# Kernel tuning notes

Measured on AMD Instinct MI355X. Metric: run time of the kernel, lower is better.

The kernel has to match this reference:

```python
import jax, jax.numpy as jnp
import numpy as np

B, C, H, W = 2, 256, 64, 64
NH = 4          # num_heads -> ch = C // NH = 64
G = 32          # GroupNorm groups (normalization(channels))
EPS = 1e-5


def setup_inputs() -> dict:
    key = jax.random.key(0)
    ks = jax.random.split(key, 7)
    s = 1.0 / np.sqrt(C).astype(np.float32)
    return {
        "x": jax.random.normal(ks[0], (B, C, H, W), jnp.float32),
        "gn_scale": 1.0 + 0.02 * jax.random.normal(ks[1], (C,), jnp.float32),
        "gn_bias": 0.02 * jax.random.normal(ks[2], (C,), jnp.float32),
        "w_qkv": s * jax.random.normal(ks[3], (3 * C, C), jnp.float32),
        "b_qkv": jnp.zeros((3 * C,), jnp.float32),
        # NOTE: original zero-inits proj_out; we use random weights so the
        # attention path contributes to the output (meaningful baseline).
        "w_proj": s * jax.random.normal(ks[4], (C, C), jnp.float32),
        "b_proj": jnp.zeros((C,), jnp.float32),
    }


def reference(x, gn_scale, gn_bias, w_qkv, b_qkv, w_proj, b_proj):
    b, c = x.shape[0], x.shape[1]
    spatial = x.shape[2:]
    t = int(np.prod(spatial))
    xf = x.reshape(b, c, t)                      # [B, C, T]

    # GroupNorm(32) over (channels-in-group, T)
    xg = xf.reshape(b, G, c // G, t)
    mu = xg.mean(axis=(2, 3), keepdims=True)
    var = xg.var(axis=(2, 3), keepdims=True)
    xn = ((xg - mu) * jax.lax.rsqrt(var + EPS)).reshape(b, c, t)
    xn = xn * gn_scale[None, :, None] + gn_bias[None, :, None]

    # 1x1 conv -> qkv: [B, 3C, T]
    qkv = jnp.einsum('oc,bct->bot', w_qkv, xn) + b_qkv[None, :, None]

    # QKVAttentionLegacy: reshape (B*H, 3*ch, T) then split
    ch = c // NH
    qkv_h = qkv.reshape(b * NH, 3 * ch, t)
    q, k, v = jnp.split(qkv_h, 3, axis=1)        # each [B*H, ch, T]
    scale = 1.0 / np.sqrt(np.sqrt(ch)).astype(np.float32)
    w = jnp.einsum('bct,bcs->bts', q * scale, k * scale)   # [B*H, T, T]
    w = jax.nn.softmax(w.astype(jnp.float32), axis=-1).astype(qkv.dtype)
    a = jnp.einsum('bts,bcs->bct', w, v).reshape(b, c, t)  # [B, C, T]

    # proj 1x1 conv + residual
    h = jnp.einsum('oc,bct->bot', w_proj, a) + b_proj[None, :, None]
    return (xf + h).reshape(b, c, *spatial)
```

## Files before the change

### kernel.cpp

```cpp
#include <hip/hip_runtime.h>
#include <math.h>

#define T 4096
#define C 256
#define BATCH 2
#define NH 4
#define G 32
#define CPG 8
#define EPS 1e-5f
#define LOG2E 1.4426950408889634f
#define QSCALE (0.125f * LOG2E)
#define KSPLIT 4
#define KRANGE (T / KSPLIT)
#define BH (BATCH * NH)

typedef __attribute__((ext_vector_type(8))) short bfv8;
typedef __attribute__((ext_vector_type(4))) short bfv4;
typedef __attribute__((ext_vector_type(4))) float f32x4;

static __device__ __forceinline__ short f2bf(float f) {
    union { float f; unsigned u; } v; v.f = f;
    return (short)((v.u + 0x7FFFu + ((v.u >> 16) & 1u)) >> 16);
}
static __device__ __forceinline__ short f2bf_fast(float f) {
    union { float f; unsigned u; } v; v.f = f;
    return (short)((v.u + 0x8000u) >> 16);
}
static __device__ __forceinline__ float bf2f(short s) {
    union { float f; unsigned u; } v; v.u = ((unsigned)(unsigned short)s) << 16;
    return v.f;
}

#if __has_builtin(__builtin_amdgcn_exp2f)
#define EXP2(x) __builtin_amdgcn_exp2f(x)
#else
#define EXP2(x) exp2f(x)
#endif

#define MFMA16(a, b, c) __builtin_amdgcn_mfma_f32_16x16x16bf16_1k(a, b, c, 0, 0, 0)

#define AS1 __attribute__((address_space(1)))
#define AS3 __attribute__((address_space(3)))
static __device__ __forceinline__ void gll16(const void* g, void* l) {
    __builtin_amdgcn_global_load_lds((const AS1 void*)g, (AS3 void*)l, 16, 0, 0);
}

__global__ __launch_bounds__(256) void prep_w(const float* __restrict__ wq,
                                              const float* __restrict__ wp,
                                              short* __restrict__ wqb,
                                              short* __restrict__ wpb) {
    int i = blockIdx.x * 256 + threadIdx.x;
    const int NQ = 768 * 256 / 4;
    float4 v; short* dst;
    if (i < NQ) { v = ((const float4*)wq)[i]; dst = wqb + i * 4; }
    else        { int j = i - NQ; v = ((const float4*)wp)[j]; dst = wpb + j * 4; }
    bfv4 o = { f2bf(v.x), f2bf(v.y), f2bf(v.z), f2bf(v.w) };
    *(bfv4*)dst = o;
}

__global__ __launch_bounds__(256) void gn_stats(const float* __restrict__ x,
                                                float* __restrict__ gnp) {
    const int blk = blockIdx.x;
    const int ts  = blockIdx.y;
    const int b = blk / G, g = blk % G;
    const float* xp = x + ((size_t)b * C + g * CPG) * T + ts * 1024;

    const int tid = threadIdx.x;
    float s = 0.f, ss = 0.f;
    #pragma unroll
    for (int u = 0; u < CPG; u++) {
        float4 v = ((const float4*)(xp + (size_t)u * T))[tid];
        s  += v.x + v.y + v.z + v.w;
        ss += v.x*v.x + v.y*v.y + v.z*v.z + v.w*v.w;
    }
    __shared__ float rs[256], rss[256];
    rs[tid] = s; rss[tid] = ss;
    __syncthreads();
    for (int off = 128; off > 0; off >>= 1) {
        if (tid < off) { rs[tid] += rs[tid+off]; rss[tid] += rss[tid+off]; }
        __syncthreads();
    }
    if (tid == 0) {
        gnp[(blk * 4 + ts) * 2 + 0] = rs[0];
        gnp[(blk * 4 + ts) * 2 + 1] = rss[0];
    }
}

__global__ __launch_bounds__(256) void gn_norm(const float* __restrict__ x,
                                               const float* __restrict__ scale,
                                               const float* __restrict__ bias,
                                               const float* __restrict__ gnp,
                                               short* __restrict__ xnT) {
    const int blk = blockIdx.x;
    const int ts  = blockIdx.y;
    const int b = blk / G, g = blk % G;
    const int c0 = g * CPG;
    const float* xp = x + ((size_t)b * C + c0) * T;

    float s = 0.f, ss = 0.f;
    #pragma unroll
    for (int i = 0; i < 4; i++) {
        s  += gnp[(blk * 4 + i) * 2 + 0];
        ss += gnp[(blk * 4 + i) * 2 + 1];
    }
    const float inv_n = 1.0f / (CPG * T);
    const float mu  = s * inv_n;
    const float var = ss * inv_n - mu * mu;
    const float rstd = rsqrtf(var + EPS);

    float sc[CPG], bi[CPG];
    #pragma unroll
    for (int u = 0; u < CPG; u++) {
        sc[u] = scale[c0+u] * rstd;
        bi[u] = bias[c0+u] - mu * sc[u];
    }

    const int t = ts * 1024 + threadIdx.x * 4;
    float vv[CPG][4];
    #pragma unroll
    for (int u = 0; u < CPG; u++) {
        float4 v = *(const float4*)&xp[(size_t)u * T + t];
        vv[u][0] = v.x * sc[u] + bi[u];
        vv[u][1] = v.y * sc[u] + bi[u];
        vv[u][2] = v.z * sc[u] + bi[u];
        vv[u][3] = v.w * sc[u] + bi[u];
    }
    #pragma unroll
    for (int j = 0; j < 4; j++) {
        bfv8 w = { f2bf(vv[0][j]), f2bf(vv[1][j]), f2bf(vv[2][j]), f2bf(vv[3][j]),
                   f2bf(vv[4][j]), f2bf(vv[5][j]), f2bf(vv[6][j]), f2bf(vv[7][j]) };
        *(bfv8*)&xnT[((size_t)b * T + t + j) * C + c0] = w;
    }
}

__global__ __launch_bounds__(256) void gemm_qkv(
    const short* __restrict__ wq,
    const float* __restrict__ bq,
    const short* __restrict__ xnT,
    short* __restrict__ qb, short* __restrict__ kb, short* __restrict__ vb)
{
    const int b  = blockIdx.z;
    const int t0 = blockIdx.x * 64;
    const int ot = blockIdx.y;
    const int h = ot / 3, part = ot % 3;
    const int o0 = ot * 64;

    __shared__ short sm[8192];
    short* Ab = sm;
    short* Bb = sm + 4096;

    const int tid = threadIdx.x, lane = tid & 63, wave = tid >> 6;
    const int col = lane & 15, quad = lane >> 4;
    const short* xb = xnT + (size_t)b * T * C;

    f32x4 acc[4];
    #pragma unroll
    for (int g = 0; g < 4; g++) { acc[g][0]=0.f; acc[g][1]=0.f; acc[g][2]=0.f; acc[g][3]=0.f; }

    for (int k0 = 0; k0 < C; k0 += 64) {
        __syncthreads();
        #pragma unroll
        for (int hh = 0; hh < 2; hh++) {
            gll16(wq + (size_t)(o0 + 16*wave + col) * C + k0 + hh*32 + quad*8,
                  Ab + (hh*4 + wave) * 512);
            gll16(xb + (size_t)(t0 + 16*wave + col) * C + k0 + hh*32 + quad*8,
                  Bb + (hh*4 + wave) * 512);
        }
        __syncthreads();
        #pragma unroll
        for (int hh = 0; hh < 2; hh++) {
            bfv8 af = *(const bfv8*)(Ab + (hh*4 + wave) * 512 + lane*8);
            #pragma unroll
            for (int g = 0; g < 4; g++) {
                bfv8 bf = *(const bfv8*)(Bb + (hh*4 + g) * 512 + lane*8);
                acc[g] = __builtin_amdgcn_mfma_f32_16x16x32_bf16(af, bf, acc[g], 0, 0, 0);
            }
        }
    }

    const int olocal = 16*wave + quad*4;
    float bias_r[4];
    #pragma unroll
    for (int r = 0; r < 4; r++) bias_r[r] = bq[o0 + olocal + r];
    const size_t hd = (size_t)(b * NH + h);

    if (part < 2) {
        short* dst = (part == 0 ? qb : kb) + hd * T * 64;
        const float sc = (part == 0) ? QSCALE : 1.0f;
        #pragma unroll
        for (int g = 0; g < 4; g++) {
            int t = t0 + 16*g + col;
            bfv4 w = { f2bf((acc[g][0] + bias_r[0]) * sc),
                       f2bf((acc[g][1] + bias_r[1]) * sc),
                       f2bf((acc[g][2] + bias_r[2]) * sc),
                       f2bf((acc[g][3] + bias_r[3]) * sc) };
            *(bfv4*)&dst[(size_t)t * 64 + olocal] = w;
        }
    } else {
        short* dst = vb + hd * 64 * T;
        #pragma unroll
        for (int g = 0; g < 4; g++)
            #pragma unroll
            for (int r = 0; r < 4; r++)
                dst[(size_t)(olocal + r) * T + t0 + 16*g + col] =
                    f2bf(acc[g][r] + bias_r[r]);
    }
}

__global__ __launch_bounds__(512, 8) void attn_kernel(
    const short* __restrict__ qb,
    const short* __restrict__ kb,
    const short* __restrict__ vb,
    short* __restrict__ opart,
    float* __restrict__ lp)
{
    __shared__ short smem[16384];
    const int bh = blockIdx.y;
    const int ks = blockIdx.z;
    const int t0 = blockIdx.x * 128;
    const int k0base = ks * KRANGE;
    const short* kbh = kb + (size_t)bh * T * 64;
    const short* vbh = vb + (size_t)bh * 64 * T;

    const int tid  = threadIdx.x;
    const int lane = tid & 63;
    const int wave = tid >> 6;
    const int col  = lane & 15;
    const int quad = lane >> 4;

    const short* qrow = qb + (size_t)bh * T * 64 + (size_t)(t0 + wave*16 + col) * 64;
    bfv8 qf0 = *(const bfv8*)(qrow + quad*8);
    bfv8 qf1 = *(const bfv8*)(qrow + 32 + quad*8);

    f32x4 oacc[4];
    #pragma unroll
    for (int g = 0; g < 4; g++) {
        oacc[g][0]=0.f; oacc[g][1]=0.f; oacc[g][2]=0.f; oacc[g][3]=0.f;
    }
    float lsum = 0.f;

    const int vq = ((quad >> 1) * 16 + col) * 8 + (quad & 1) * 4;

    const int kg = wave & 3, hi = wave >> 2;
    #define STAGE_KV(buf, s0)                                                  \
        {                                                                      \
            short* base = smem + (buf) * 8192;                                 \
            gll16(kbh + (size_t)((s0) + 16*kg + col) * 64 + (quad + 4*hi)*8,   \
                  base + wave * 512);                                          \
            gll16(vbh + (size_t)(16*kg + col) * T + (s0) + (quad + 4*hi)*8,    \
                  base + 4096 + wave * 512);                                   \
        }

    STAGE_KV(0, k0base)

    for (int it = 0; it < KRANGE/64; it++) {
        __syncthreads();
        if (it + 1 < KRANGE/64) STAGE_KV((it+1) & 1, k0base + (it+1)*64)

        const short* kvb = smem + (it & 1) * 8192;

        bfv4 pf[4];
        #pragma unroll
        for (int g = 0; g < 4; g++) {
            bfv8 kf0 = *(const bfv8*)(kvb + g*512 + lane*8);
            bfv8 kf1 = *(const bfv8*)(kvb + (4+g)*512 + lane*8);
            f32x4 a;
            a[0]=0.f; a[1]=0.f; a[2]=0.f; a[3]=0.f;
            a = __builtin_amdgcn_mfma_f32_16x16x32_bf16(kf0, qf0, a, 0, 0, 0);
            a = __builtin_amdgcn_mfma_f32_16x16x32_bf16(kf1, qf1, a, 0, 0, 0);
            #pragma unroll
            for (int r = 0; r < 4; r++) {
                float p = EXP2(a[r]);
                lsum += p;
                pf[g][r] = f2bf_fast(p);
            }
        }

        const short* vbase = kvb + 4096;
        #pragma unroll
        for (int g = 0; g < 4; g++) {
            bfv4 v0 = *(const bfv4*)(vbase + g*512 + vq);
            bfv4 v1 = *(const bfv4*)(vbase + g*512 + vq + 256);
            bfv4 v2 = *(const bfv4*)(vbase + (4+g)*512 + vq);
            bfv4 v3 = *(const bfv4*)(vbase + (4+g)*512 + vq + 256);
            oacc[g] = MFMA16(v0, pf[0], oacc[g]);
            oacc[g] = MFMA16(v1, pf[1], oacc[g]);
            oacc[g] = MFMA16(v2, pf[2], oacc[g]);
            oacc[g] = MFMA16(v3, pf[3], oacc[g]);
        }
    }

    lsum += __shfl_xor(lsum, 16);
    lsum += __shfl_xor(lsum, 32);

    const size_t rowbase = (size_t)(ks*BH + bh) * T + t0 + wave*16;
    short* opb = opart + (rowbase + col) * 64;
    #pragma unroll
    for (int g = 0; g < 4; g++) {
        bfv4 w = { f2bf(oacc[g][0]), f2bf(oacc[g][1]),
                   f2bf(oacc[g][2]), f2bf(oacc[g][3]) };
        *(bfv4*)(opb + 16*g + quad*4) = w;
    }
    if (lane < 16) {
        lp[rowbase + col] = lsum;
    }
}

__global__ __launch_bounds__(256) void gemm_proj(
    const short* __restrict__ wp,
    const float* __restrict__ bp,
    const short* __restrict__ opart,
    const float* __restrict__ lp,
    const float* __restrict__ x,
    float* __restrict__ out)
{
    const int b  = blockIdx.z;
    const int t0 = blockIdx.x * 64;
    const int o0 = blockIdx.y * 64;

    __shared__ short sm[8192];
    short* Ab = sm;
    short* Bb = sm + 4096;

    const int tid = threadIdx.x, lane = tid & 63, wave = tid >> 6;
    const int col = lane & 15, quad = lane >> 4;

    const int trow = t0 + 16*wave + col;
    float rl4[NH];
    #pragma unroll
    for (int hh = 0; hh < NH; hh++) {
        float ls = 0.f;
        #pragma unroll
        for (int ks = 0; ks < KSPLIT; ks++)
            ls += lp[((size_t)(ks*BH) + b*NH + hh) * T + trow];
        rl4[hh] = 1.0f / ls;
    }

    f32x4 acc[4];
    #pragma unroll
    for (int g = 0; g < 4; g++) { acc[g][0]=0.f; acc[g][1]=0.f; acc[g][2]=0.f; acc[g][3]=0.f; }

    for (int k0 = 0; k0 < C; k0 += 64) {
        __syncthreads();
        #pragma unroll
        for (int hh = 0; hh < 2; hh++) {
            gll16(wp + (size_t)(o0 + 16*wave + col) * C + k0 + hh*32 + quad*8,
                  Ab + (hh*4 + wave) * 512);
            const int chg = k0 + hh*32 + quad*8;
            const int hd = chg >> 6, chin = chg & 63;
            const short* ob = opart + (((size_t)(b*NH + hd)) * T + trow) * 64 + chin;
            float a8[8] = {0.f,0.f,0.f,0.f,0.f,0.f,0.f,0.f};
            #pragma unroll
            for (int ks = 0; ks < KSPLIT; ks++) {
                bfv8 v = *(const bfv8*)(ob + (size_t)ks * BH * T * 64);
                #pragma unroll
                for (int u = 0; u < 8; u++) a8[u] += bf2f(v[u]);
            }
            const float rl = rl4[hd];
            bfv8 pk;
            #pragma unroll
            for (int u = 0; u < 8; u++) pk[u] = f2bf(a8[u] * rl);
            *(bfv8*)(Bb + (hh*4 + wave) * 512 + lane*8) = pk;
        }
        __syncthreads();
        #pragma unroll
        for (int hh = 0; hh < 2; hh++) {
            bfv8 af = *(const bfv8*)(Ab + (hh*4 + wave) * 512 + lane*8);
            #pragma unroll
            for (int g = 0; g < 4; g++) {
                bfv8 bf = *(const bfv8*)(Bb + (hh*4 + g) * 512 + lane*8);
                acc[g] = __builtin_amdgcn_mfma_f32_16x16x32_bf16(af, bf, acc[g], 0, 0, 0);
            }
        }
    }

    const int olocal = 16*wave + quad*4;
    #pragma unroll
    for (int r = 0; r < 4; r++) {
        const int o = o0 + olocal + r;
        const float bias = bp[o];
        const size_t rowoff = ((size_t)b * C + o) * T;
        #pragma unroll
        for (int g = 0; g < 4; g++) {
            const size_t idx = rowoff + t0 + 16*g + col;
            out[idx] = acc[g][r] + bias + x[idx];
        }
    }
}

extern "C" void kernel_launch(void* const* d_in, const int* in_sizes, int n_in,
                              void* d_out, int out_size, void* d_ws, size_t ws_size,
                              hipStream_t stream) {
    (void)in_sizes; (void)n_in; (void)out_size; (void)ws_size;
    const float* x        = (const float*)d_in[0];
    const float* gn_scale = (const float*)d_in[1];
    const float* gn_bias  = (const float*)d_in[2];
    const float* w_qkv    = (const float*)d_in[3];
    const float* b_qkv    = (const float*)d_in[4];
    const float* w_proj   = (const float*)d_in[5];
    const float* b_proj   = (const float*)d_in[6];
    float* out = (float*)d_out;

    short* ws    = (short*)d_ws;
    short* qb    = ws;
    short* kb    = qb  + (size_t)BH * T * 64;
    short* vb    = kb  + (size_t)BH * T * 64;
    short* xnT   = vb  + (size_t)BH * T * 64;
    short* wqb   = xnT + (size_t)BATCH * T * C;
    short* wpb   = wqb + 768 * 256;
    short* opart = wpb + 256 * 256;
    float* lp    = (float*)(opart + (size_t)KSPLIT * BH * T * 64);
    float* gnp   = lp + (size_t)KSPLIT * BH * T;

    prep_w<<<dim3(256), 256, 0, stream>>>(w_qkv, w_proj, wqb, wpb);
    gn_stats<<<dim3(BATCH * G, 4), 256, 0, stream>>>(x, gnp);
    gn_norm<<<dim3(BATCH * G, 4), 256, 0, stream>>>(x, gn_scale, gn_bias, gnp, xnT);
    gemm_qkv<<<dim3(T/64, 12, BATCH), 256, 0, stream>>>(wqb, b_qkv, xnT, qb, kb, vb);
    attn_kernel<<<dim3(T/128, BH, KSPLIT), 512, 0, stream>>>(qb, kb, vb, opart, lp);
    gemm_proj<<<dim3(T/64, 4, BATCH), 256, 0, stream>>>(wpb, b_proj, opart, lp, x, out);
}
```

Baseline: 158.0 us.

## Switch attention kernel to 32x32x16 MFMA with 256-query tiles and swizzled LDS

Rewrites the attention inner loop to use 32x32x16 bf16 MFMA instructions, so each wave handles 32 query rows instead of 16 and each block covers 256 queries instead of 128. Each K/V tile staged into LDS is therefore reused across twice as many queries, halving the global K/V traffic per query. The LDS layout gets an XOR swizzle to avoid bank conflicts with the new access pattern. In exchange, the grid has half as many blocks, register pressure is higher, and launch bounds drop the occupancy target from 8 to 4.

```diff
diff --git a/kernel.cpp b/kernel.cpp
--- a/kernel.cpp
+++ b/kernel.cpp
@@ -17,6 +17,7 @@
 typedef __attribute__((ext_vector_type(8))) short bfv8;
 typedef __attribute__((ext_vector_type(4))) short bfv4;
 typedef __attribute__((ext_vector_type(4))) float f32x4;
+typedef __attribute__((ext_vector_type(16))) float f32x16;
 
 static __device__ __forceinline__ short f2bf(float f) {
     union { float f; unsigned u; } v; v.f = f;
@@ -36,8 +37,6 @@
 #else
 #define EXP2(x) exp2f(x)
 #endif
-
-#define MFMA16(a, b, c) __builtin_amdgcn_mfma_f32_16x16x16bf16_1k(a, b, c, 0, 0, 0)
 
 #define AS1 __attribute__((address_space(1)))
 #define AS3 __attribute__((address_space(3)))
@@ -207,7 +206,7 @@
     }
 }
 
-__global__ __launch_bounds__(512, 8) void attn_kernel(
+__global__ __launch_bounds__(512, 4) void attn_kernel(
     const short* __restrict__ qb,
     const short* __restrict__ kb,
     const short* __restrict__ vb,
@@ -217,7 +216,7 @@
     __shared__ short smem[16384];
     const int bh = blockIdx.y;
     const int ks = blockIdx.z;
-    const int t0 = blockIdx.x * 128;
+    const int t0 = blockIdx.x * 256;
     const int k0base = ks * KRANGE;
     const short* kbh = kb + (size_t)bh * T * 64;
     const short* vbh = vb + (size_t)bh * 64 * T;
@@ -225,30 +224,32 @@
     const int tid  = threadIdx.x;
     const int lane = tid & 63;
     const int wave = tid >> 6;
-    const int col  = lane & 15;
-    const int quad = lane >> 4;
-
-    const short* qrow = qb + (size_t)bh * T * 64 + (size_t)(t0 + wave*16 + col) * 64;
-    bfv8 qf0 = *(const bfv8*)(qrow + quad*8);
-    bfv8 qf1 = *(const bfv8*)(qrow + 32 + quad*8);
-
-    f32x4 oacc[4];
-    #pragma unroll
-    for (int g = 0; g < 4; g++) {
-        oacc[g][0]=0.f; oacc[g][1]=0.f; oacc[g][2]=0.f; oacc[g][3]=0.f;
-    }
+    const int klow = lane & 31;
+    const int hi   = lane >> 5;
+    const int swz  = klow & 7;
+
+    const int q = t0 + wave*32 + klow;
+    const short* qrow = qb + (size_t)bh * T * 64 + (size_t)q * 64;
+    bfv8 qf[4];
+    #pragma unroll
+    for (int s = 0; s < 4; s++) qf[s] = *(const bfv8*)(qrow + s*16 + hi*8);
+
+    f32x16 oacc[2];
+    #pragma unroll
+    for (int c = 0; c < 2; c++)
+        #pragma unroll
+        for (int r = 0; r < 16; r++) oacc[c][r] = 0.f;
     float lsum = 0.f;
 
-    const int vq = ((quad >> 1) * 16 + col) * 8 + (quad & 1) * 4;
-
-    const int kg = wave & 3, hi = wave >> 2;
-    #define STAGE_KV(buf, s0)                                                  \
-        {                                                                      \
-            short* base = smem + (buf) * 8192;                                 \
-            gll16(kbh + (size_t)((s0) + 16*kg + col) * 64 + (quad + 4*hi)*8,   \
-                  base + wave * 512);                                          \
-            gll16(vbh + (size_t)(16*kg + col) * T + (s0) + (quad + 4*hi)*8,    \
-                  base + 4096 + wave * 512);                                   \
+    const int srow = wave*8 + (lane >> 3);
+    const int schunk = lane & 7;
+    #define STAGE_KV(buf, s0)                                                   \
+        {                                                                       \
+            short* kB = smem + (buf) * 8192 + wave * 512;                       \
+            gll16(kbh + (size_t)((s0) + srow) * 64 + ((schunk ^ (srow&7))<<3),  \
+                  kB);                                                          \
+            gll16(vbh + (size_t)srow * T + (s0) + ((schunk ^ (srow&7))<<3),     \
+                  kB + 4096);                                                   \
         }
 
     STAGE_KV(0, k0base)
@@ -258,51 +259,61 @@
         if (it + 1 < KRANGE/64) STAGE_KV((it+1) & 1, k0base + (it+1)*64)
 
         const short* kvb = smem + (it & 1) * 8192;
-
-        bfv4 pf[4];
-        #pragma unroll
-        for (int g = 0; g < 4; g++) {
-            bfv8 kf0 = *(const bfv8*)(kvb + g*512 + lane*8);
-            bfv8 kf1 = *(const bfv8*)(kvb + (4+g)*512 + lane*8);
-            f32x4 a;
-            a[0]=0.f; a[1]=0.f; a[2]=0.f; a[3]=0.f;
-            a = __builtin_amdgcn_mfma_f32_16x16x32_bf16(kf0, qf0, a, 0, 0, 0);
-            a = __builtin_amdgcn_mfma_f32_16x16x32_bf16(kf1, qf1, a, 0, 0, 0);
-            #pragma unroll
-            for (int r = 0; r < 4; r++) {
-                float p = EXP2(a[r]);
-                lsum += p;
-                pf[g][r] = f2bf_fast(p);
-            }
-        }
-
-        const short* vbase = kvb + 4096;
-        #pragma unroll
-        for (int g = 0; g < 4; g++) {
-            bfv4 v0 = *(const bfv4*)(vbase + g*512 + vq);
-            bfv4 v1 = *(const bfv4*)(vbase + g*512 + vq + 256);
-            bfv4 v2 = *(const bfv4*)(vbase + (4+g)*512 + vq);
-            bfv4 v3 = *(const bfv4*)(vbase + (4+g)*512 + vq + 256);
-            oacc[g] = MFMA16(v0, pf[0], oacc[g]);
-            oacc[g] = MFMA16(v1, pf[1], oacc[g]);
-            oacc[g] = MFMA16(v2, pf[2], oacc[g]);
-            oacc[g] = MFMA16(v3, pf[3], oacc[g]);
-        }
-    }
-
-    lsum += __shfl_xor(lsum, 16);
+        const short* kl = kvb + klow*64;
+        const short* vl = kvb + 4096 + klow*64 + 4*hi;
+
+        bfv8 pf[2][2];
+        #pragma unroll
+        for (int kt = 0; kt < 2; kt++) {
+            f32x16 sacc;
+            #pragma unroll
+            for (int r = 0; r < 16; r++) sacc[r] = 0.f;
+            #pragma unroll
+            for (int s = 0; s < 4; s++) {
+                bfv8 kf = *(const bfv8*)(kl + kt*2048 + (((2*s+hi) ^ swz) << 3));
+                sacc = __builtin_amdgcn_mfma_f32_32x32x16_bf16(kf, qf[s], sacc, 0, 0, 0);
+            }
+            #pragma unroll
+            for (int u = 0; u < 2; u++) {
+                bfv8 pk;
+                #pragma unroll
+                for (int j = 0; j < 8; j++) {
+                    float p = EXP2(sacc[u*8 + j]);
+                    lsum += p;
+                    pk[j] = f2bf_fast(p);
+                }
+                pf[kt][u] = pk;
+            }
+        }
+
+        #pragma unroll
+        for (int kc = 0; kc < 4; kc++) {
+            #pragma unroll
+            for (int c = 0; c < 2; c++) {
+                bfv4 v0 = *(const bfv4*)(vl + c*2048 + (((2*kc)   ^ swz) << 3));
+                bfv4 v1 = *(const bfv4*)(vl + c*2048 + (((2*kc+1) ^ swz) << 3));
+                bfv8 vf = { v0[0], v0[1], v0[2], v0[3],
+                            v1[0], v1[1], v1[2], v1[3] };
+                oacc[c] = __builtin_amdgcn_mfma_f32_32x32x16_bf16(
+                              vf, pf[kc>>1][kc&1], oacc[c], 0, 0, 0);
+            }
+        }
+    }
+
     lsum += __shfl_xor(lsum, 32);
 
-    const size_t rowbase = (size_t)(ks*BH + bh) * T + t0 + wave*16;
-    short* opb = opart + (rowbase + col) * 64;
-    #pragma unroll
-    for (int g = 0; g < 4; g++) {
-        bfv4 w = { f2bf(oacc[g][0]), f2bf(oacc[g][1]),
-                   f2bf(oacc[g][2]), f2bf(oacc[g][3]) };
-        *(bfv4*)(opb + 16*g + quad*4) = w;
-    }
-    if (lane < 16) {
-        lp[rowbase + col] = lsum;
+    const size_t rowbase = (size_t)(ks*BH + bh) * T + t0 + wave*32;
+    short* opb = opart + (rowbase + klow) * 64;
+    #pragma unroll
+    for (int c = 0; c < 2; c++)
+        #pragma unroll
+        for (int u = 0; u < 4; u++) {
+            bfv4 w = { f2bf(oacc[c][4*u+0]), f2bf(oacc[c][4*u+1]),
+                       f2bf(oacc[c][4*u+2]), f2bf(oacc[c][4*u+3]) };
+            *(bfv4*)(opb + c*32 + u*8 + hi*4) = w;
+        }
+    if (hi == 0) {
+        lp[rowbase + klow] = lsum;
     }
 }
 
@@ -416,6 +427,6 @@
     gn_stats<<<dim3(BATCH * G, 4), 256, 0, stream>>>(x, gnp);
     gn_norm<<<dim3(BATCH * G, 4), 256, 0, stream>>>(x, gn_scale, gn_bias, gnp, xnT);
     gemm_qkv<<<dim3(T/64, 12, BATCH), 256, 0, stream>>>(wqb, b_qkv, xnT, qb, kb, vb);
-    attn_kernel<<<dim3(T/128, BH, KSPLIT), 512, 0, stream>>>(qb, kb, vb, opart, lp);
+    attn_kernel<<<dim3(T/256, BH, KSPLIT), 512, 0, stream>>>(qb, kb, vb, opart, lp);
     gemm_proj<<<dim3(T/64, 4, BATCH), 256, 0, stream>>>(wpb, b_proj, opart, lp, x, out);
 }
```

New measurement: 152.4 us. -3.6%, faster.
